# Optimization experiments

Hardware: AMD Instinct MI355X
Metric: run time of the kernel (lower is better)

## Reference

```python
import jax, jax.numpy as jnp
import numpy as np

NUM_EXPERTS = 8
D_IN = 2048
D_OUT = 8192
TOKENS = 8192
# ragged per-expert token counts (sum == TOKENS), imbalanced on purpose
EXPERT_SIZES = [512, 1536, 768, 1280, 1024, 1024, 896, 1152]


def setup_inputs() -> dict:
    key = jax.random.key(0)
    k1, k2 = jax.random.split(key)
    inputs = jax.random.normal(k1, (TOKENS, D_IN), dtype=jnp.float32)
    bound = 1.0 / D_IN  # matches nn.init.uniform_(-1/in, 1/in)
    weight = jax.random.uniform(k2, (NUM_EXPERTS, D_IN, D_OUT),
                                minval=-bound, maxval=bound, dtype=jnp.float32)
    expert_size = np.array(EXPERT_SIZES, dtype=np.int64)  # static split sizes
    return {"inputs": inputs, "weight": weight, "expert_size": expert_size}


def reference(inputs, weight, expert_size):
    # Grouped GEMM: tokens are pre-sorted by expert; expert_size gives the
    # contiguous token count per expert. Sizes are static (host ints), so the
    # per-expert loop has fixed shapes and is jit-friendly.
    sizes = [int(s) for s in np.asarray(expert_size)]
    offs = np.cumsum([0] + sizes)
    outs = [inputs[offs[i]:offs[i + 1]] @ weight[i]  # [n_i, D_IN] @ [D_IN, D_OUT]
            for i in range(len(sizes))]
    return jnp.concatenate(outs, axis=0)  # [TOKENS, D_OUT]
```

## Files before the change

### kernel.cpp

```cpp
#include <hip/hip_runtime.h>
#include <hip/hip_bf16.h>

#define NE   8
#define DIN  2048
#define DOUT 8192
#define NTOK 8192

typedef __bf16 bf16;
typedef __attribute__((ext_vector_type(8))) __bf16 bf16x8;
typedef __attribute__((ext_vector_type(4))) float f32x4;

__device__ __forceinline__ bf16 f2bf(float x) {
  union { float f; unsigned u; } v; v.f = x;
  unsigned r = v.u + 0x7fffu + ((v.u >> 16) & 1u);
  union { unsigned short s; bf16 b; } o; o.s = (unsigned short)(r >> 16);
  return o.b;
}

__device__ __forceinline__ int find_expert(const void* esv, int mrow) {
  const int* p32 = (const int*)esv;
  const long long* p64 = (const long long*)esv;
  bool is64 = (p32[1] == 0);
  long long cum = 0; int e = 0;
  #pragma unroll
  for (int i = 0; i < NE; ++i) {
    long long s = is64 ? p64[i] : (long long)p32[i];
    long long nx = cum + s;
    if ((long long)mrow >= nx) e = i + 1;
    cum = nx;
  }
  return e;
}

__global__ __launch_bounds__(256) void convertA(const float* __restrict__ A,
                                                bf16* __restrict__ Ab) {
  size_t i = ((size_t)blockIdx.x * 256 + threadIdx.x) * 8;
  float4 a = *(const float4*)(A + i);
  float4 b = *(const float4*)(A + i + 4);
  const float* f = (const float*)&a;
  const float* g = (const float*)&b;
  bf16x8 v;
  #pragma unroll
  for (int j = 0; j < 4; ++j) { v[j] = f2bf(f[j]); v[4 + j] = f2bf(g[j]); }
  *(bf16x8*)(Ab + i) = v;
}

__global__ __launch_bounds__(256) void convertB(const float* __restrict__ W,
                                                bf16* __restrict__ BT) {
  __shared__ bf16 tile[64][66];
  const int e  = blockIdx.z;
  const int n0 = blockIdx.x * 64;
  const int k0 = blockIdx.y * 64;
  const int t  = threadIdx.x;
  const int tr = t >> 2;
  const int tc = (t & 3) << 4;

  const float* src = W + ((size_t)e * DIN + k0 + tr) * DOUT + n0 + tc;
  #pragma unroll
  for (int i = 0; i < 4; ++i) {
    float4 v = *(const float4*)(src + 4 * i);
    const float* f = (const float*)&v;
    #pragma unroll
    for (int j = 0; j < 4; ++j) tile[tr][tc + 4 * i + j] = f2bf(f[j]);
  }
  __syncthreads();

  bf16x8 v0, v1;
  #pragma unroll
  for (int j = 0; j < 8; ++j) { v0[j] = tile[tc + j][tr]; v1[j] = tile[tc + 8 + j][tr]; }
  bf16* dst = BT + ((size_t)e * DOUT + n0 + tr) * DIN + k0 + tc;
  *(bf16x8*)dst = v0;
  *(bf16x8*)(dst + 8) = v1;
}

#define BM 128
#define BN 128
#define BK 64

#define GL(gp, lp) __builtin_amdgcn_global_load_lds(                        \
    (const __attribute__((address_space(1))) void*)(gp),                    \
    (__attribute__((address_space(3))) void*)(lp), 16, 0, 0)

__global__ __launch_bounds__(256) void grouped_gemm(
    const bf16* __restrict__ A, const bf16* __restrict__ BT,
    const void* __restrict__ es, float* __restrict__ C) {
  __shared__ bf16 As[BM * BK];
  __shared__ bf16 Bs[BN * BK];

  const int bid   = blockIdx.x;
  const int c     = bid & 7;
  const int local = bid >> 3;
  const int mtile = local >> 3;
  const int ntile = c * 8 + (local & 7);
  const int mrow  = mtile * BM;
  const int ncol  = ntile * BN;
  const int e     = find_expert(es, mrow);

  const int t    = threadIdx.x;
  const int lane = t & 63;
  const int wr   = ((t >> 6) >> 1) * 64;
  const int wc   = ((t >> 6) & 1) * 64;
  const int l15  = lane & 15;
  const int kg   = lane >> 4;

  const int srow = t >> 3;
  const int ssrc = ((t & 7) ^ ((t >> 3) & 7)) * 8;
  const int sdst = t * 8;

  const bf16* Ag = A + (size_t)(mrow + srow) * DIN + ssrc;
  const bf16* Bg = BT + ((size_t)e * DOUT + ncol + srow) * DIN + ssrc;

  f32x4 acc[4][4];
  #pragma unroll
  for (int m = 0; m < 4; ++m)
    #pragma unroll
    for (int n = 0; n < 4; ++n) acc[m][n] = (f32x4){0.f, 0.f, 0.f, 0.f};

  const int rc0 = ((0 * 4 + kg) ^ (l15 & 7)) * 8;
  const int rc1 = ((1 * 4 + kg) ^ (l15 & 7)) * 8;

  for (int kt = 0; kt < DIN / BK; ++kt) {
    const int kb = kt * BK;
    #pragma unroll
    for (int i = 0; i < 4; ++i) {
      GL(Ag + (size_t)(i * 32) * DIN + kb, As + i * 2048 + sdst);
      GL(Bg + (size_t)(i * 32) * DIN + kb, Bs + i * 2048 + sdst);
    }
    __syncthreads();

    #pragma unroll
    for (int kk = 0; kk < 2; ++kk) {
      const int rc = kk ? rc1 : rc0;
      bf16x8 af[4], bfr[4];
      #pragma unroll
      for (int m = 0; m < 4; ++m)
        af[m] = *(const bf16x8*)&As[(wr + m * 16 + l15) * BK + rc];
      #pragma unroll
      for (int n = 0; n < 4; ++n)
        bfr[n] = *(const bf16x8*)&Bs[(wc + n * 16 + l15) * BK + rc];
      #pragma unroll
      for (int m = 0; m < 4; ++m)
        #pragma unroll
        for (int n = 0; n < 4; ++n)
          acc[m][n] = __builtin_amdgcn_mfma_f32_16x16x32_bf16(
              af[m], bfr[n], acc[m][n], 0, 0, 0);
    }
    __syncthreads();
  }

  float* Cb = C + (size_t)mrow * DOUT + ncol;
  const int r0 = wr + kg * 4;
  const int c0 = wc + l15;
  #pragma unroll
  for (int m = 0; m < 4; ++m)
    #pragma unroll
    for (int j = 0; j < 4; ++j)
      #pragma unroll
      for (int n = 0; n < 4; ++n)
        Cb[(size_t)(r0 + m * 16 + j) * DOUT + c0 + n * 16] = acc[m][n][j];
}

__global__ __launch_bounds__(256) void fallback_gemm(
    const float* __restrict__ A, const float* __restrict__ W,
    const void* __restrict__ es, float* __restrict__ C) {
  __shared__ float Asf[64][17];
  __shared__ float Bsf[16][65];
  const int bid = blockIdx.x;
  const int mtile = bid >> 7;
  const int ntile = bid & 127;
  const int mrow = mtile * 64, ncol = ntile * 64;
  const int e = find_expert(es, mrow);
  const int t = threadIdx.x;
  const int tx = t & 15, ty = t >> 4;
  float acc[4][4] = {};
  const float* Ab = A + (size_t)mrow * DIN;
  const float* Wb = W + (size_t)e * DIN * DOUT + ncol;
  for (int kb = 0; kb < DIN; kb += 16) {
    {
      const int r = t >> 2, c = (t & 3) * 4;
      float4 v = *(const float4*)(Ab + (size_t)r * DIN + kb + c);
      const float* f = (const float*)&v;
      #pragma unroll
      for (int j = 0; j < 4; ++j) Asf[r][c + j] = f[j];
      const int r2 = t >> 4, c2 = (t & 15) * 4;
      float4 wv = *(const float4*)(Wb + (size_t)(kb + r2) * DOUT + c2);
      const float* g = (const float*)&wv;
      #pragma unroll
      for (int j = 0; j < 4; ++j) Bsf[r2][c2 + j] = g[j];
    }
    __syncthreads();
    #pragma unroll
    for (int k = 0; k < 16; ++k)
      #pragma unroll
      for (int i = 0; i < 4; ++i)
        #pragma unroll
        for (int j = 0; j < 4; ++j)
          acc[i][j] += Asf[ty * 4 + i][k] * Bsf[k][tx * 4 + j];
    __syncthreads();
  }
  #pragma unroll
  for (int i = 0; i < 4; ++i)
    #pragma unroll
    for (int j = 0; j < 4; ++j)
      C[(size_t)(mrow + ty * 4 + i) * DOUT + ncol + tx * 4 + j] = acc[i][j];
}

extern "C" void kernel_launch(void* const* d_in, const int* in_sizes, int n_in,
                              void* d_out, int out_size, void* d_ws, size_t ws_size,
                              hipStream_t stream) {
  const float* A = (const float*)d_in[0];
  const float* W = (const float*)d_in[1];
  const void*  es = (const void*)d_in[2];
  float* C = (float*)d_out;

  const size_t needA = (size_t)NTOK * DIN * sizeof(bf16);
  const size_t needB = (size_t)NE * DIN * DOUT * sizeof(bf16);

  if (ws_size >= needA + needB) {
    bf16* Ab = (bf16*)d_ws;
    bf16* BT = (bf16*)((char*)d_ws + needA);
    convertA<<<(NTOK * DIN) / (256 * 8), 256, 0, stream>>>(A, Ab);
    dim3 gB(DOUT / 64, DIN / 64, NE);
    convertB<<<gB, 256, 0, stream>>>(W, BT);
    grouped_gemm<<<(NTOK / BM) * (DOUT / BN), 256, 0, stream>>>(Ab, BT, es, C);
  } else {
    fallback_gemm<<<(NTOK / 64) * (DOUT / 64), 256, 0, stream>>>(A, W, es, C);
  }
}
```

Measured before the change: 508.3 us.

## Fuse weight fp32-to-bf16 conversion and transpose into grouped GEMM B-tile loads

Drops the separate convertB pass, which converted and transposed all 8 expert weight matrices (512 MB of fp32 read, 256 MB of bf16 written), and has the GEMM read fp32 weights directly. Each thread loads eight K-rows of float4, converts them to bf16 in registers and writes transposed, swizzled bf16x8 vectors into LDS. The block-to-tile mapping is also changed so consecutive blocks walk M tiles within an N-column group, which should help L2 reuse of the weight tiles. The trade-off is that B is now loaded synchronously through registers rather than with global_load_lds, and weight bytes are re-read in fp32 by every M tile, doubling that traffic per tile.

```diff
diff --git a/kernel.cpp b/kernel.cpp
--- a/kernel.cpp
+++ b/kernel.cpp
@@ -45,34 +45,6 @@
   *(bf16x8*)(Ab + i) = v;
 }
 
-__global__ __launch_bounds__(256) void convertB(const float* __restrict__ W,
-                                                bf16* __restrict__ BT) {
-  __shared__ bf16 tile[64][66];
-  const int e  = blockIdx.z;
-  const int n0 = blockIdx.x * 64;
-  const int k0 = blockIdx.y * 64;
-  const int t  = threadIdx.x;
-  const int tr = t >> 2;
-  const int tc = (t & 3) << 4;
-
-  const float* src = W + ((size_t)e * DIN + k0 + tr) * DOUT + n0 + tc;
-  #pragma unroll
-  for (int i = 0; i < 4; ++i) {
-    float4 v = *(const float4*)(src + 4 * i);
-    const float* f = (const float*)&v;
-    #pragma unroll
-    for (int j = 0; j < 4; ++j) tile[tr][tc + 4 * i + j] = f2bf(f[j]);
-  }
-  __syncthreads();
-
-  bf16x8 v0, v1;
-  #pragma unroll
-  for (int j = 0; j < 8; ++j) { v0[j] = tile[tc + j][tr]; v1[j] = tile[tc + 8 + j][tr]; }
-  bf16* dst = BT + ((size_t)e * DOUT + n0 + tr) * DIN + k0 + tc;
-  *(bf16x8*)dst = v0;
-  *(bf16x8*)(dst + 8) = v1;
-}
-
 #define BM 128
 #define BN 128
 #define BK 64
@@ -82,7 +54,7 @@
     (__attribute__((address_space(3))) void*)(lp), 16, 0, 0)
 
 __global__ __launch_bounds__(256) void grouped_gemm(
-    const bf16* __restrict__ A, const bf16* __restrict__ BT,
+    const bf16* __restrict__ A, const float* __restrict__ W,
     const void* __restrict__ es, float* __restrict__ C) {
   __shared__ bf16 As[BM * BK];
   __shared__ bf16 Bs[BN * BK];
@@ -90,8 +62,8 @@
   const int bid   = blockIdx.x;
   const int c     = bid & 7;
   const int local = bid >> 3;
-  const int mtile = local >> 3;
-  const int ntile = c * 8 + (local & 7);
+  const int mtile = local & 63;
+  const int ntile = c * 8 + (local >> 6);
   const int mrow  = mtile * BM;
   const int ncol  = ntile * BN;
   const int e     = find_expert(es, mrow);
@@ -104,40 +76,69 @@
   const int kg   = lane >> 4;
 
   const int srow = t >> 3;
-  const int ssrc = ((t & 7) ^ ((t >> 3) & 7)) * 8;
+  const int ssrc = ((t & 7) ^ (srow & 7)) * 8;
   const int sdst = t * 8;
-
   const bf16* Ag = A + (size_t)(mrow + srow) * DIN + ssrc;
-  const bf16* Bg = BT + ((size_t)e * DOUT + ncol + srow) * DIN + ssrc;
+
+  const int tn4 = (t & 31) * 4;
+  const int tk  = t >> 5;
+  const float* Wg = W + (size_t)e * DIN * DOUT + (size_t)(tk * 8) * DOUT + ncol + tn4;
+  char* BsB = (char*)Bs;
 
   f32x4 acc[4][4];
   #pragma unroll
   for (int m = 0; m < 4; ++m)
     #pragma unroll
     for (int n = 0; n < 4; ++n) acc[m][n] = (f32x4){0.f, 0.f, 0.f, 0.f};
-
-  const int rc0 = ((0 * 4 + kg) ^ (l15 & 7)) * 8;
-  const int rc1 = ((1 * 4 + kg) ^ (l15 & 7)) * 8;
 
   for (int kt = 0; kt < DIN / BK; ++kt) {
     const int kb = kt * BK;
+
+    float4 wv0 = *(const float4*)(Wg + (size_t)(kb + 0) * DOUT);
+    float4 wv1 = *(const float4*)(Wg + (size_t)(kb + 1) * DOUT);
+    float4 wv2 = *(const float4*)(Wg + (size_t)(kb + 2) * DOUT);
+    float4 wv3 = *(const float4*)(Wg + (size_t)(kb + 3) * DOUT);
+    float4 wv4 = *(const float4*)(Wg + (size_t)(kb + 4) * DOUT);
+    float4 wv5 = *(const float4*)(Wg + (size_t)(kb + 5) * DOUT);
+    float4 wv6 = *(const float4*)(Wg + (size_t)(kb + 6) * DOUT);
+    float4 wv7 = *(const float4*)(Wg + (size_t)(kb + 7) * DOUT);
+
+    #pragma unroll
+    for (int i = 0; i < 4; ++i)
+      GL(Ag + (size_t)(i * 32) * DIN + kb, As + i * 2048 + sdst);
+
     #pragma unroll
     for (int i = 0; i < 4; ++i) {
-      GL(Ag + (size_t)(i * 32) * DIN + kb, As + i * 2048 + sdst);
-      GL(Bg + (size_t)(i * 32) * DIN + kb, Bs + i * 2048 + sdst);
+      bf16x8 bv;
+      bv[0] = (bf16)(((const float*)&wv0)[i]);
+      bv[1] = (bf16)(((const float*)&wv1)[i]);
+      bv[2] = (bf16)(((const float*)&wv2)[i]);
+      bv[3] = (bf16)(((const float*)&wv3)[i]);
+      bv[4] = (bf16)(((const float*)&wv4)[i]);
+      bv[5] = (bf16)(((const float*)&wv5)[i]);
+      bv[6] = (bf16)(((const float*)&wv6)[i]);
+      bv[7] = (bf16)(((const float*)&wv7)[i]);
+      const int row  = tn4 + i;
+      const int slot = tk ^ ((row & 7) ^ ((row >> 3) & 7));
+      *(bf16x8*)(BsB + row * 128 + slot * 16) = bv;
     }
+
     __syncthreads();
 
     #pragma unroll
     for (int kk = 0; kk < 2; ++kk) {
-      const int rc = kk ? rc1 : rc0;
+      const int rcA = ((kk * 4 + kg) ^ (l15 & 7)) * 8;
       bf16x8 af[4], bfr[4];
       #pragma unroll
       for (int m = 0; m < 4; ++m)
-        af[m] = *(const bf16x8*)&As[(wr + m * 16 + l15) * BK + rc];
-      #pragma unroll
-      for (int n = 0; n < 4; ++n)
-        bfr[n] = *(const bf16x8*)&Bs[(wc + n * 16 + l15) * BK + rc];
+        af[m] = *(const bf16x8*)&As[(wr + m * 16 + l15) * BK + rcA];
+      #pragma unroll
+      for (int n = 0; n < 4; ++n) {
+        const int row = wc + n * 16 + l15;
+        const int g   = (kk * 4 + kg) ^ (l15 & 7) ^
+                        (((wc >> 3) + 2 * n + (l15 >> 3)) & 7);
+        bfr[n] = *(const bf16x8*)(BsB + row * 128 + g * 16);
+      }
       #pragma unroll
       for (int m = 0; m < 4; ++m)
         #pragma unroll
@@ -177,11 +178,11 @@
   const float* Wb = W + (size_t)e * DIN * DOUT + ncol;
   for (int kb = 0; kb < DIN; kb += 16) {
     {
-      const int r = t >> 2, c = (t & 3) * 4;
-      float4 v = *(const float4*)(Ab + (size_t)r * DIN + kb + c);
+      const int r = t >> 2, cc = (t & 3) * 4;
+      float4 v = *(const float4*)(Ab + (size_t)r * DIN + kb + cc);
       const float* f = (const float*)&v;
       #pragma unroll
-      for (int j = 0; j < 4; ++j) Asf[r][c + j] = f[j];
+      for (int j = 0; j < 4; ++j) Asf[r][cc + j] = f[j];
       const int r2 = t >> 4, c2 = (t & 15) * 4;
       float4 wv = *(const float4*)(Wb + (size_t)(kb + r2) * DOUT + c2);
       const float* g = (const float*)&wv;
@@ -214,15 +215,11 @@
   float* C = (float*)d_out;
 
   const size_t needA = (size_t)NTOK * DIN * sizeof(bf16);
-  const size_t needB = (size_t)NE * DIN * DOUT * sizeof(bf16);
-
-  if (ws_size >= needA + needB) {
+
+  if (ws_size >= needA) {
     bf16* Ab = (bf16*)d_ws;
-    bf16* BT = (bf16*)((char*)d_ws + needA);
     convertA<<<(NTOK * DIN) / (256 * 8), 256, 0, stream>>>(A, Ab);
-    dim3 gB(DOUT / 64, DIN / 64, NE);
-    convertB<<<gB, 256, 0, stream>>>(W, BT);
-    grouped_gemm<<<(NTOK / BM) * (DOUT / BN), 256, 0, stream>>>(Ab, BT, es, C);
+    grouped_gemm<<<(NTOK / BM) * (DOUT / BN), 256, 0, stream>>>(Ab, W, es, C);
   } else {
     fallback_gemm<<<(NTOK / 64) * (DOUT / 64), 256, 0, stream>>>(A, W, es, C);
   }
```

After: 537.7 us. +5.8%, slower.
